# Kernel optimization log

Measured on AMD Instinct MI355X. Metric: run time of the kernel, lower is better.

The kernel has to match this reference:

```python
import jax, jax.numpy as jnp
import numpy as np

N = 100000       # nodes
E0 = 1600000     # edges without self loops
E = E0 + N       # with self loops appended (attr 0), matching add_self_loops
DIN = 128        # input_dim
HID = 64         # nb_hidden_gnn (per-head out_channels)
HEADS = 4
EMB = 128
L = 3            # nb_layer
NEG_SLOPE = 0.2
BN_EPS = 1e-5


def setup_inputs() -> dict:
    key = jax.random.key(0)
    ks = jax.random.split(key, 12)
    # edges with no self loops; self loops (i,i) appended with edge_attr 0
    row = jax.random.randint(ks[0], (E0,), 0, N)
    off = jax.random.randint(ks[1], (E0,), 1, N)
    col = (row + off) % N
    loops = jnp.arange(N, dtype=row.dtype)
    edge_index = jnp.stack([jnp.concatenate([row, loops]),
                            jnp.concatenate([col, loops])])
    edge_attr = jnp.concatenate([jax.random.normal(ks[2], (E0, 1), jnp.float32),
                                 jnp.zeros((N, 1), jnp.float32)])
    x = jax.random.normal(ks[3], (N, DIN), jnp.float32)
    HC = HEADS * HID
    linN0 = jax.random.normal(ks[4], (DIN, HC)) * HC ** -0.5
    linN_rest = jax.random.normal(ks[5], (L - 1, HID, HC)) * HC ** -0.5
    linE_all = jax.random.normal(ks[6], (L, 1, HEADS)) * HEADS ** -0.5  # nb_edge_attr=1
    att_all = jax.random.normal(ks[7], (L, HEADS, 2 * HID + 1)) * (2 * HID + 1) ** -0.5
    bias_all = jnp.zeros((L, HID))  # concat=False -> bias [out_channels]
    bn_gamma = jnp.ones((L - 1, HID))
    bn_beta = jnp.zeros((L - 1, HID))
    W = jax.random.normal(ks[8], (HID, EMB)) * HID ** -0.5
    b = jnp.zeros((EMB,))
    return {"x": x, "edge_index": edge_index, "edge_attr": edge_attr,
            "linN0": linN0, "linN_rest": linN_rest, "linE_all": linE_all,
            "att_all": att_all, "bias_all": bias_all,
            "bn_gamma": bn_gamma, "bn_beta": bn_beta, "W": W, "b": b}


def _gcn_layer(x, row, col, edge_attr, linN, linE, att, bias, bn):
    n = x.shape[0]
    if bn is not None:
        gamma, beta = bn
        mu = x.mean(axis=0)
        var = x.var(axis=0)
        x = (x - mu) * jax.lax.rsqrt(var + BN_EPS) * gamma + beta
    h = (x @ linN).reshape(n, HEADS, HID)                 # [N,H,C]
    e = (edge_attr @ linE)                                # [E,H] (nb_edge_attr=1)
    att_i = att[:, :HID]                                  # [H,C]
    att_j = att[:, HID:2 * HID]                           # [H,C]
    att_e = att[:, 2 * HID:]                              # [H,1]
    # per-node partial scores avoid gathering full features twice
    s_i = jnp.einsum('nhc,hc->nh', h, att_i)
    s_j = jnp.einsum('nhc,hc->nh', h, att_j)
    logits = s_i[row] + s_j[col] + e * att_e[:, 0]        # [E,H]
    logits = jax.nn.leaky_relu(logits, NEG_SLOPE)
    # segment softmax over destination nodes (edge_index[1])
    m = jax.ops.segment_max(logits, col, num_segments=n)
    p = jnp.exp(logits - m[col])
    denom = jax.ops.segment_sum(p, col, num_segments=n)
    alpha = p / (denom[col] + 1e-16)
    # message: alpha * x[source], scatter-add to destination
    msg = alpha[:, :, None] * h[row]                      # [E,H,C]
    out = jax.ops.segment_sum(msg, col, num_segments=n)   # [N,H,C]
    out = out.mean(axis=1) + bias + h.mean(axis=1)        # concat=False, res=True
    return jax.nn.relu(out)


def reference(x, edge_index, edge_attr, linN0, linN_rest, linE_all, att_all,
              bias_all, bn_gamma, bn_beta, W, b):
    row, col = edge_index[0], edge_index[1]
    emb = x
    for l in range(L):
        linN = linN0 if l == 0 else linN_rest[l - 1]
        bn = None if l == 0 else (bn_gamma[l - 1], bn_beta[l - 1])
        emb = _gcn_layer(emb, row, col, edge_attr, linN, linE_all[l],
                         att_all[l], bias_all[l], bn)
    return emb @ W + b
```

## Files before the change

kernel.cpp:

```cpp
#include <hip/hip_runtime.h>
#include <math.h>

#define NN 100000
#define E0E 1600000
#define EE (E0E + NN)
#define NEG 0.2f
#define BNEPS 1e-5f
#define LOG2E 1.4426950408889634f

typedef float f4 __attribute__((ext_vector_type(4)));
typedef float f2 __attribute__((ext_vector_type(2)));
typedef short s8v __attribute__((ext_vector_type(8)));

__device__ __forceinline__ float wred_max(float v) {
#pragma unroll
  for (int m = 1; m < 64; m <<= 1) v = fmaxf(v, __shfl_xor(v, m, 64));
  return v;
}
__device__ __forceinline__ float wred_sum(float v) {
#pragma unroll
  for (int m = 1; m < 64; m <<= 1) v += __shfl_xor(v, m, 64);
  return v;
}
__device__ __forceinline__ float sel4(float a0, float a1, float a2, float a3, int hd) {
  return (hd & 2) ? ((hd & 1) ? a3 : a2) : ((hd & 1) ? a1 : a0);
}
__device__ __forceinline__ unsigned short f2bf(float x) {
  unsigned u = __float_as_uint(x);
  return (unsigned short)((u + 0x7fffu + ((u >> 16) & 1u)) >> 16);
}
__device__ __forceinline__ float bf2f(unsigned short s) {
  return __uint_as_float(((unsigned)s) << 16);
}

__global__ void k_init(int* cnt, double* bnsum, int n) {
  int i = blockIdx.x * blockDim.x + threadIdx.x;
  if (i < n) cnt[i] = 0;
  if (i < 256) bnsum[i] = 0.0;
}
__global__ void k_count(const int* __restrict__ col, int* cnt, int e) {
  int i = blockIdx.x * blockDim.x + threadIdx.x;
  if (i < e) atomicAdd(&cnt[col[i]], 1);
}
#define SCAN_T 1024
__global__ void k_scan1(const int* __restrict__ cnt, int* partial, int n, int chunk) {
  int i = blockIdx.x * blockDim.x + threadIdx.x;
  int beg = i * chunk, end = min(n, beg + chunk);
  int s = 0;
  for (int j = beg; j < end; ++j) s += cnt[j];
  partial[i] = s;
}
__global__ void k_scan2(int* partial) {
  __shared__ int lds[SCAN_T];
  int t = threadIdx.x;
  int v = partial[t];
  lds[t] = v;
  __syncthreads();
  for (int off = 1; off < SCAN_T; off <<= 1) {
    int add = (t >= off) ? lds[t - off] : 0;
    __syncthreads();
    lds[t] += add;
    __syncthreads();
  }
  partial[t] = lds[t] - v;
}
__global__ void k_scan3(const int* __restrict__ cnt, const int* __restrict__ partial,
                        int* rowptr, int* cursor, int n, int chunk, int etot) {
  int i = blockIdx.x * blockDim.x + threadIdx.x;
  int beg = i * chunk, end = min(n, beg + chunk);
  int run = partial[i];
  for (int j = beg; j < end; ++j) {
    rowptr[j] = run;
    cursor[j] = run;
    run += cnt[j];
  }
  if (i == SCAN_T - 1) rowptr[n] = etot;
}
__global__ void k_scatter(const int* __restrict__ row, const int* __restrict__ col,
                          const float* __restrict__ ea, int* cursor, int2* csr, int e) {
  int i = blockIdx.x * blockDim.x + threadIdx.x;
  if (i < e) {
    int c = col[i];
    int p = atomicAdd(&cursor[c], 1);
    csr[p] = make_int2(row[i], __float_as_int(ea[i]));
  }
}

__global__ void k_bnstats(const float* __restrict__ x, double* sums, int n) {
  int f = threadIdx.x & 63;
  int rt = (blockIdx.x * blockDim.x + threadIdx.x) >> 6;
  int rstride = (gridDim.x * blockDim.x) >> 6;
  double s = 0.0, q = 0.0;
  for (int r = rt; r < n; r += rstride) {
    double v = (double)x[(size_t)r * 64 + f];
    s += v;
    q += v * v;
  }
  __shared__ double ls[256], lq[256];
  ls[threadIdx.x] = s;
  lq[threadIdx.x] = q;
  __syncthreads();
  if (threadIdx.x < 64) {
    s = ls[threadIdx.x] + ls[threadIdx.x + 64] + ls[threadIdx.x + 128] + ls[threadIdx.x + 192];
    q = lq[threadIdx.x] + lq[threadIdx.x + 64] + lq[threadIdx.x + 128] + lq[threadIdx.x + 192];
    atomicAdd(&sums[f], s);
    atomicAdd(&sums[64 + f], q);
  }
}

__global__ void k_prepw(const float* __restrict__ W, const double* __restrict__ bnsum,
                        const float* __restrict__ gamma, const float* __restrict__ beta,
                        const float* __restrict__ bin, unsigned short* __restrict__ Wt,
                        float* __restrict__ cvec, int K, int N, int mode) {
  __shared__ float ABl[128];
  int t = threadIdx.x;
  if (mode == 1) {
    if (t < 64) {
      double mean = bnsum[t] / NN;
      double var = bnsum[64 + t] / NN - mean * mean;
      float A = gamma[t] * rsqrtf((float)var + BNEPS);
      ABl[t] = A;
      ABl[64 + t] = beta[t] - (float)mean * A;
    }
    __syncthreads();
  }
  if (t >= N) return;
  float c = (mode == 2) ? bin[t] : 0.f;
  for (int k = 0; k < K; ++k) {
    float w = W[k * N + t];
    float a = 1.f, b = 0.f;
    if (mode == 1) { a = ABl[k]; b = ABl[64 + k]; }
    Wt[t * K + k] = f2bf(a * w);
    c = fmaf(b, w, c);
  }
  cvec[t] = c;
}

template <int K, int CT, bool ATT, bool OB>
__global__ __launch_bounds__(256, 2) void k_gemm(const float* __restrict__ x,
                                                 const unsigned short* __restrict__ Wt,
                                                 const float* __restrict__ cvec,
                                                 const float* __restrict__ att,
                                                 void* __restrict__ houtv,
                                                 float* __restrict__ s_i,
                                                 float* __restrict__ s_j, int n,
                                                 int ntiles) {
  constexpr int KS = K / 32;
  constexpr int ROWB = 2 * K;
  constexpr int CPR = K / 8;
  constexpr int NCOL = 4 * CT * 16;
  __shared__ unsigned char xs[64 * ROWB];
  const int lane = threadIdx.x & 63;
  const int wv = threadIdx.x >> 6;
  const int l15 = lane & 15;
  const int lq = lane >> 4;
  const int colbase = wv * CT * 16;

  s8v wfr[CT][KS];
#pragma unroll
  for (int ct = 0; ct < CT; ++ct)
#pragma unroll
    for (int ks = 0; ks < KS; ++ks)
      wfr[ct][ks] = *(const s8v*)&Wt[(size_t)(colbase + ct * 16 + l15) * K + ks * 32 + lq * 8];
  float cb[CT][4];
#pragma unroll
  for (int ct = 0; ct < CT; ++ct)
#pragma unroll
    for (int r = 0; r < 4; ++r) cb[ct][r] = cvec[colbase + ct * 16 + lq * 4 + r];
  float ati[ATT ? CT : 1][4], atj[ATT ? CT : 1][4];
  if constexpr (ATT) {
    const float* ar = att + wv * 129;
#pragma unroll
    for (int ct = 0; ct < CT; ++ct)
#pragma unroll
      for (int r = 0; r < 4; ++r) {
        int cc = ct * 16 + lq * 4 + r;
        ati[ct][r] = ar[cc];
        atj[ct][r] = ar[64 + cc];
      }
  }

  for (int t = blockIdx.x; t < ntiles; t += gridDim.x) {
    const int row0 = t * 64;
    __syncthreads();
#pragma unroll
    for (int i = 0; i < (64 * CPR) / 256; ++i) {
      int c = threadIdx.x + i * 256;
      int row = c / CPR, kc = c % CPR;
      int rg = min(row0 + row, n - 1);
      const float* xp = x + (size_t)rg * K + kc * 8;
      f4 a0 = *(const f4*)xp;
      f4 a1 = *(const f4*)(xp + 4);
      union { s8v v; unsigned short u[8]; } pk;
      pk.u[0] = f2bf(a0[0]); pk.u[1] = f2bf(a0[1]); pk.u[2] = f2bf(a0[2]); pk.u[3] = f2bf(a0[3]);
      pk.u[4] = f2bf(a1[0]); pk.u[5] = f2bf(a1[1]); pk.u[6] = f2bf(a1[2]); pk.u[7] = f2bf(a1[3]);
      *(s8v*)&xs[row * ROWB + ((kc * 16) ^ ((row & 7) << 4))] = pk.v;
    }
    __syncthreads();
    f4 acc[4][CT];
#pragma unroll
    for (int rt = 0; rt < 4; ++rt)
#pragma unroll
      for (int ct = 0; ct < CT; ++ct) acc[rt][ct] = (f4)0.f;
#pragma unroll
    for (int ks = 0; ks < KS; ++ks) {
      s8v xf[4];
#pragma unroll
      for (int rt = 0; rt < 4; ++rt) {
        int row = rt * 16 + l15;
        int kb = ks * 64 + lq * 16;
        xf[rt] = *(const s8v*)&xs[row * ROWB + (kb ^ ((row & 7) << 4))];
      }
#pragma unroll
      for (int rt = 0; rt < 4; ++rt)
#pragma unroll
        for (int ct = 0; ct < CT; ++ct)
          acc[rt][ct] = __builtin_amdgcn_mfma_f32_16x16x32_bf16(wfr[ct][ks], xf[rt],
                                                                acc[rt][ct], 0, 0, 0);
    }
#pragma unroll
    for (int rt = 0; rt < 4; ++rt) {
      if (row0 + rt * 16 >= n) continue;
      const size_t xrow = (size_t)(row0 + rt * 16 + l15);
      float v[CT][4];
#pragma unroll
      for (int ct = 0; ct < CT; ++ct)
#pragma unroll
        for (int r = 0; r < 4; ++r) v[ct][r] = acc[rt][ct][r] + cb[ct][r];
      if constexpr (OB) {
        float* outp = (float*)houtv;
#pragma unroll
        for (int ct = 0; ct < CT; ++ct) {
          f4 o;
          o[0] = v[ct][0]; o[1] = v[ct][1]; o[2] = v[ct][2]; o[3] = v[ct][3];
          *(f4*)&outp[xrow * NCOL + colbase + ct * 16 + lq * 4] = o;
        }
      } else {
        unsigned short* hout = (unsigned short*)houtv;
#pragma unroll
        for (int ct = 0; ct < CT; ++ct) {
          ushort4 hb4;
          hb4.x = f2bf(v[ct][0]); hb4.y = f2bf(v[ct][1]);
          hb4.z = f2bf(v[ct][2]); hb4.w = f2bf(v[ct][3]);
          *(ushort4*)&hout[xrow * NCOL + colbase + ct * 16 + lq * 4] = hb4;
        }
      }
      if constexpr (ATT) {
        float pi = 0.f, pj = 0.f;
#pragma unroll
        for (int ct = 0; ct < CT; ++ct)
#pragma unroll
          for (int r = 0; r < 4; ++r) {
            pi = fmaf(v[ct][r], ati[ct][r], pi);
            pj = fmaf(v[ct][r], atj[ct][r], pj);
          }
        pi += __shfl_xor(pi, 16, 64); pi += __shfl_xor(pi, 32, 64);
        pj += __shfl_xor(pj, 16, 64); pj += __shfl_xor(pj, 32, 64);
        if (lane < 16) {
          s_i[xrow * 4 + wv] = pi;
          s_j[xrow * 4 + wv] = pj;
        }
      }
    }
  }
}

template <int UNR>
__global__ __launch_bounds__(256) void k_edge(const int* __restrict__ rowptr,
                                              const int2* __restrict__ csr,
                                              const float* __restrict__ s_i,
                                              const float* __restrict__ s_j,
                                              const unsigned short* __restrict__ hb,
                                              const float* __restrict__ linE,
                                              const float* __restrict__ att,
                                              const float* __restrict__ bias,
                                              float* __restrict__ xout, int n) {
  __shared__ float lp[4][64][4];
  __shared__ int lsrc[4][64];
  const int lane = threadIdx.x & 63;
  const int wid = threadIdx.x >> 6;
  int v = blockIdx.x * 4 + wid;
  if (v >= n) return;
  v = __builtin_amdgcn_readfirstlane(v);
  const int base = rowptr[v];
  const int deg = rowptr[v + 1] - base;

  const float coef0 = linE[0] * att[0 * 129 + 128];
  const float coef1 = linE[1] * att[1 * 129 + 128];
  const float coef2 = linE[2] * att[2 * 129 + 128];
  const float coef3 = linE[3] * att[3 * 129 + 128];
  const float sj0 = s_j[(size_t)v * 4 + 0];
  const float sj1 = s_j[(size_t)v * 4 + 1];
  const float sj2 = s_j[(size_t)v * 4 + 2];
  const float sj3 = s_j[(size_t)v * 4 + 3];

  auto edge_logits = [&](int i, int& src, float& g0, float& g1, float& g2, float& g3) {
    int2 pk = csr[i];
    src = pk.x;
    float ea = __int_as_float(pk.y);
    f4 siv = *(const f4*)&s_i[(size_t)src * 4];
    g0 = siv[0] + sj0 + ea * coef0; g0 = fmaxf(g0, g0 * NEG);
    g1 = siv[1] + sj1 + ea * coef1; g1 = fmaxf(g1, g1 * NEG);
    g2 = siv[2] + sj2 + ea * coef2; g2 = fmaxf(g2, g2 * NEG);
    g3 = siv[3] + sj3 + ea * coef3; g3 = fmaxf(g3, g3 * NEG);
  };

  const int hd = lane >> 4;
  float msel, rdsel;
  bool fast = (deg <= 64);
  if (fast) {
    float g0 = -INFINITY, g1 = -INFINITY, g2 = -INFINITY, g3 = -INFINITY;
    int src = 0;
    bool valid = lane < deg;
    if (valid) edge_logits(base + lane, src, g0, g1, g2, g3);
    float m0 = wred_max(g0), m1 = wred_max(g1), m2 = wred_max(g2), m3 = wred_max(g3);
    float p0 = valid ? exp2f((g0 - m0) * LOG2E) : 0.f;
    float p1 = valid ? exp2f((g1 - m1) * LOG2E) : 0.f;
    float p2 = valid ? exp2f((g2 - m2) * LOG2E) : 0.f;
    float p3 = valid ? exp2f((g3 - m3) * LOG2E) : 0.f;
    if (valid) {
      f4 pp; pp[0] = p0; pp[1] = p1; pp[2] = p2; pp[3] = p3;
      *(f4*)&lp[wid][lane][0] = pp;
      lsrc[wid][lane] = src;
    }
    float d0 = wred_sum(p0), d1 = wred_sum(p1), d2 = wred_sum(p2), d3 = wred_sum(p3);
    rdsel = 1.f / (sel4(d0, d1, d2, d3, hd) + 1e-16f);
    msel = 0.f;
  } else {
    float m0 = -INFINITY, m1 = -INFINITY, m2 = -INFINITY, m3 = -INFINITY;
    for (int c0 = 0; c0 < deg; c0 += 64) {
      int i = c0 + lane;
      if (i < deg) {
        int src; float g0, g1, g2, g3;
        edge_logits(base + i, src, g0, g1, g2, g3);
        m0 = fmaxf(m0, g0); m1 = fmaxf(m1, g1); m2 = fmaxf(m2, g2); m3 = fmaxf(m3, g3);
      }
    }
    m0 = wred_max(m0); m1 = wred_max(m1); m2 = wred_max(m2); m3 = wred_max(m3);
    float d0 = 0, d1 = 0, d2 = 0, d3 = 0;
    for (int c0 = 0; c0 < deg; c0 += 64) {
      int i = c0 + lane;
      if (i < deg) {
        int src; float g0, g1, g2, g3;
        edge_logits(base + i, src, g0, g1, g2, g3);
        d0 += exp2f((g0 - m0) * LOG2E);
        d1 += exp2f((g1 - m1) * LOG2E);
        d2 += exp2f((g2 - m2) * LOG2E);
        d3 += exp2f((g3 - m3) * LOG2E);
      }
    }
    d0 = wred_sum(d0); d1 = wred_sum(d1); d2 = wred_sum(d2); d3 = wred_sum(d3);
    msel = sel4(m0, m1, m2, m3, hd);
    rdsel = 1.f / (sel4(d0, d1, d2, d3, hd) + 1e-16f);
  }

  f4 acc;
  {
    ushort4 hr = *(const ushort4*)&hb[(size_t)v * 256 + lane * 4];
    acc[0] = bf2f(hr.x); acc[1] = bf2f(hr.y); acc[2] = bf2f(hr.z); acc[3] = bf2f(hr.w);
  }
  if (fast) {
    int e = 0;
    if constexpr (UNR > 1) {
      for (; e + UNR <= deg; e += UNR) {
        int ss[UNR];
        float aa[UNR];
        ushort4 hh[UNR];
#pragma unroll
        for (int u = 0; u < UNR; ++u) {
          ss[u] = lsrc[wid][e + u];
          aa[u] = lp[wid][e + u][hd] * rdsel;
        }
#pragma unroll
        for (int u = 0; u < UNR; ++u)
          hh[u] = *(const ushort4*)&hb[(size_t)ss[u] * 256 + lane * 4];
#pragma unroll
        for (int u = 0; u < UNR; ++u) {
          acc[0] = fmaf(aa[u], bf2f(hh[u].x), acc[0]);
          acc[1] = fmaf(aa[u], bf2f(hh[u].y), acc[1]);
          acc[2] = fmaf(aa[u], bf2f(hh[u].z), acc[2]);
          acc[3] = fmaf(aa[u], bf2f(hh[u].w), acc[3]);
        }
      }
    }
    for (; e < deg; ++e) {
      int s0 = lsrc[wid][e];
      float a0 = lp[wid][e][hd] * rdsel;
      ushort4 h0 = *(const ushort4*)&hb[(size_t)s0 * 256 + lane * 4];
      acc[0] = fmaf(a0, bf2f(h0.x), acc[0]);
      acc[1] = fmaf(a0, bf2f(h0.y), acc[1]);
      acc[2] = fmaf(a0, bf2f(h0.z), acc[2]);
      acc[3] = fmaf(a0, bf2f(h0.w), acc[3]);
    }
  } else {
    const float sjsel = sel4(sj0, sj1, sj2, sj3, hd);
    const float cfsel = sel4(coef0, coef1, coef2, coef3, hd);
    for (int e = base; e < base + deg; ++e) {
      int2 pk = csr[e];
      int src = pk.x;
      float ea = __int_as_float(pk.y);
      f4 siv = *(const f4*)&s_i[(size_t)src * 4];
      float lg = sel4(siv[0], siv[1], siv[2], siv[3], hd) + sjsel + ea * cfsel;
      lg = fmaxf(lg, lg * NEG);
      float a = exp2f((lg - msel) * LOG2E) * rdsel;
      ushort4 hr = *(const ushort4*)&hb[(size_t)src * 256 + lane * 4];
      acc[0] = fmaf(a, bf2f(hr.x), acc[0]);
      acc[1] = fmaf(a, bf2f(hr.y), acc[1]);
      acc[2] = fmaf(a, bf2f(hr.z), acc[2]);
      acc[3] = fmaf(a, bf2f(hr.w), acc[3]);
    }
  }
#pragma unroll
  for (int m = 16; m < 64; m <<= 1) {
    acc[0] += __shfl_xor(acc[0], m, 64);
    acc[1] += __shfl_xor(acc[1], m, 64);
    acc[2] += __shfl_xor(acc[2], m, 64);
    acc[3] += __shfl_xor(acc[3], m, 64);
  }
  if (lane < 16) {
    f4 bv = *(const f4*)&bias[lane * 4];
    f4 o;
#pragma unroll
    for (int c = 0; c < 4; ++c) o[c] = fmaxf(acc[c] * 0.25f + bv[c], 0.f);
    *(f4*)&xout[(size_t)v * 64 + lane * 4] = o;
  }
}

extern "C" void kernel_launch(void* const* d_in, const int* in_sizes, int n_in,
                              void* d_out, int out_size, void* d_ws, size_t ws_size,
                              hipStream_t stream) {
  const float* x_in = (const float*)d_in[0];
  const int* ei = (const int*)d_in[1];
  const float* eattr = (const float*)d_in[2];
  const float* linN0 = (const float*)d_in[3];
  const float* linNr = (const float*)d_in[4];
  const float* linE = (const float*)d_in[5];
  const float* attA = (const float*)d_in[6];
  const float* biasA = (const float*)d_in[7];
  const float* bng = (const float*)d_in[8];
  const float* bnb = (const float*)d_in[9];
  const float* W = (const float*)d_in[10];
  const float* bb = (const float*)d_in[11];
  float* out = (float*)d_out;

  const int* row = ei;
  const int* col = ei + EE;

  char* ws = (char*)d_ws;
  size_t o = 0;
  auto alloc = [&](size_t bytes) {
    void* p = ws + o;
    o += (bytes + 255) & ~(size_t)255;
    return p;
  };
  int* cnt = (int*)alloc((size_t)NN * 4);
  int* cursor = (int*)alloc((size_t)NN * 4);
  int* rowptr = (int*)alloc((size_t)(NN + 1) * 4);
  int* partial = (int*)alloc((size_t)SCAN_T * 4);
  int2* csr = (int2*)alloc((size_t)EE * 8);
  unsigned short* h = (unsigned short*)alloc((size_t)NN * 256 * 2);
  float* si = (float*)alloc((size_t)NN * 4 * 4);
  float* sj = (float*)alloc((size_t)NN * 4 * 4);
  float* xa = (float*)alloc((size_t)NN * 64 * 4);
  float* xb = (float*)alloc((size_t)NN * 64 * 4);
  double* bnsum = (double*)alloc(256 * 8);
  unsigned short* Wt = (unsigned short*)alloc((size_t)256 * 128 * 2);
  float* cvec = (float*)alloc(256 * 4);
  if (o > ws_size) return;

  const int chunk = (NN + SCAN_T - 1) / SCAN_T;
  const int NTILES = (NN + 63) / 64;

  k_init<<<(NN + 255) / 256, 256, 0, stream>>>(cnt, bnsum, NN);
  k_count<<<(EE + 255) / 256, 256, 0, stream>>>(col, cnt, EE);
  k_scan1<<<4, 256, 0, stream>>>(cnt, partial, NN, chunk);
  k_scan2<<<1, SCAN_T, 0, stream>>>(partial);
  k_scan3<<<4, 256, 0, stream>>>(cnt, partial, rowptr, cursor, NN, chunk, EE);
  k_scatter<<<(EE + 255) / 256, 256, 0, stream>>>(row, col, eattr, cursor, csr, EE);

  k_prepw<<<1, 256, 0, stream>>>(linN0, nullptr, nullptr, nullptr, nullptr, Wt, cvec, 128, 256, 0);
  k_gemm<128, 4, true, false><<<NTILES, 256, 0, stream>>>(x_in, Wt, cvec, attA + 0, h, si, sj,
                                                          NN, NTILES);
  k_edge<4><<<NN / 4, 256, 0, stream>>>(rowptr, csr, si, sj, h, linE + 0, attA + 0, biasA + 0,
                                        xa, NN);

  k_bnstats<<<256, 256, 0, stream>>>(xa, bnsum, NN);
  k_prepw<<<1, 256, 0, stream>>>(linNr, bnsum, bng, bnb, nullptr, Wt, cvec, 64, 256, 1);
  k_gemm<64, 4, true, false><<<NTILES, 256, 0, stream>>>(xa, Wt, cvec, attA + 516, h, si, sj,
                                                         NN, NTILES);
  k_edge<2><<<NN / 4, 256, 0, stream>>>(rowptr, csr, si, sj, h, linE + 4, attA + 516, biasA + 64,
                                        xb, NN);

  k_bnstats<<<256, 256, 0, stream>>>(xb, bnsum + 128, NN);
  k_prepw<<<1, 256, 0, stream>>>(linNr + 64 * 256, bnsum + 128, bng + 64, bnb + 64, nullptr,
                                 Wt, cvec, 64, 256, 1);
  k_gemm<64, 4, true, false><<<NTILES, 256, 0, stream>>>(xb, Wt, cvec, attA + 2 * 516, h, si, sj,
                                                         NN, NTILES);
  k_edge<1><<<NN / 4, 256, 0, stream>>>(rowptr, csr, si, sj, h, linE + 8, attA + 2 * 516,
                                        biasA + 128, xa, NN);

  k_prepw<<<1, 256, 0, stream>>>(W, nullptr, nullptr, nullptr, bb, Wt, cvec, 64, 128, 2);
  k_gemm<64, 2, false, true><<<NTILES, 256, 0, stream>>>(xa, Wt, cvec, nullptr, out, nullptr,
                                                         nullptr, NN, NTILES);
}
```

Before: 904.6 us.

## Store intermediate activations in bf16, restructure edge kernel, parallelize weight prep

```diff
diff --git a/kernel.cpp b/kernel.cpp
--- a/kernel.cpp
+++ b/kernel.cpp
@@ -86,13 +86,13 @@
   }
 }
 
-__global__ void k_bnstats(const float* __restrict__ x, double* sums, int n) {
+__global__ void k_bnstats(const unsigned short* __restrict__ x, double* sums, int n) {
   int f = threadIdx.x & 63;
   int rt = (blockIdx.x * blockDim.x + threadIdx.x) >> 6;
   int rstride = (gridDim.x * blockDim.x) >> 6;
   double s = 0.0, q = 0.0;
   for (int r = rt; r < n; r += rstride) {
-    double v = (double)x[(size_t)r * 64 + f];
+    double v = (double)bf2f(x[(size_t)r * 64 + f]);
     s += v;
     q += v * v;
   }
@@ -113,6 +113,7 @@
                         const float* __restrict__ bin, unsigned short* __restrict__ Wt,
                         float* __restrict__ cvec, int K, int N, int mode) {
   __shared__ float ABl[128];
+  __shared__ float cred[4][64];
   int t = threadIdx.x;
   if (mode == 1) {
     if (t < 64) {
@@ -124,20 +125,30 @@
     }
     __syncthreads();
   }
-  if (t >= N) return;
-  float c = (mode == 2) ? bin[t] : 0.f;
-  for (int k = 0; k < K; ++k) {
-    float w = W[k * N + t];
+  int cl = t & 63, kq = t >> 6;
+  int col = blockIdx.x * 64 + cl;
+  int kn = K >> 2;
+  int k0 = kq * kn;
+  float c = 0.f;
+#pragma unroll 8
+  for (int k = k0; k < k0 + kn; ++k) {
+    float w = W[k * N + col];
     float a = 1.f, b = 0.f;
     if (mode == 1) { a = ABl[k]; b = ABl[64 + k]; }
-    Wt[t * K + k] = f2bf(a * w);
+    Wt[col * K + k] = f2bf(a * w);
     c = fmaf(b, w, c);
   }
-  cvec[t] = c;
-}
-
-template <int K, int CT, bool ATT, bool OB>
-__global__ __launch_bounds__(256, 2) void k_gemm(const float* __restrict__ x,
+  cred[kq][cl] = c;
+  __syncthreads();
+  if (kq == 0) {
+    float cc = cred[0][cl] + cred[1][cl] + cred[2][cl] + cred[3][cl];
+    if (mode == 2) cc += bin[col];
+    cvec[col] = cc;
+  }
+}
+
+template <int K, int CT, bool ATT, bool OB, bool INBF>
+__global__ __launch_bounds__(256, 2) void k_gemm(const void* __restrict__ xv,
                                                  const unsigned short* __restrict__ Wt,
                                                  const float* __restrict__ cvec,
                                                  const float* __restrict__ att,
@@ -188,13 +199,20 @@
       int c = threadIdx.x + i * 256;
       int row = c / CPR, kc = c % CPR;
       int rg = min(row0 + row, n - 1);
-      const float* xp = x + (size_t)rg * K + kc * 8;
-      f4 a0 = *(const f4*)xp;
-      f4 a1 = *(const f4*)(xp + 4);
-      union { s8v v; unsigned short u[8]; } pk;
-      pk.u[0] = f2bf(a0[0]); pk.u[1] = f2bf(a0[1]); pk.u[2] = f2bf(a0[2]); pk.u[3] = f2bf(a0[3]);
-      pk.u[4] = f2bf(a1[0]); pk.u[5] = f2bf(a1[1]); pk.u[6] = f2bf(a1[2]); pk.u[7] = f2bf(a1[3]);
-      *(s8v*)&xs[row * ROWB + ((kc * 16) ^ ((row & 7) << 4))] = pk.v;
+      int dst = row * ROWB + ((kc * 16) ^ ((row & 7) << 4));
+      if constexpr (INBF) {
+        const unsigned short* xin = (const unsigned short*)xv;
+        *(s8v*)&xs[dst] = *(const s8v*)&xin[(size_t)rg * K + kc * 8];
+      } else {
+        const float* xin = (const float*)xv;
+        const float* xp = xin + (size_t)rg * K + kc * 8;
+        f4 a0 = *(const f4*)xp;
+        f4 a1 = *(const f4*)(xp + 4);
+        union { s8v v; unsigned short u[8]; } pk;
+        pk.u[0] = f2bf(a0[0]); pk.u[1] = f2bf(a0[1]); pk.u[2] = f2bf(a0[2]); pk.u[3] = f2bf(a0[3]);
+        pk.u[4] = f2bf(a1[0]); pk.u[5] = f2bf(a1[1]); pk.u[6] = f2bf(a1[2]); pk.u[7] = f2bf(a1[3]);
+        *(s8v*)&xs[dst] = pk.v;
+      }
     }
     __syncthreads();
     f4 acc[4][CT];
@@ -265,7 +283,6 @@
   }
 }
 
-template <int UNR>
 __global__ __launch_bounds__(256) void k_edge(const int* __restrict__ rowptr,
                                               const int2* __restrict__ csr,
                                               const float* __restrict__ s_i,
@@ -274,11 +291,13 @@
                                               const float* __restrict__ linE,
                                               const float* __restrict__ att,
                                               const float* __restrict__ bias,
-                                              float* __restrict__ xout, int n) {
+                                              unsigned short* __restrict__ xout, int n) {
   __shared__ float lp[4][64][4];
   __shared__ int lsrc[4][64];
+  const unsigned char* hb8 = (const unsigned char*)hb;
   const int lane = threadIdx.x & 63;
   const int wid = threadIdx.x >> 6;
+  const int lane8 = lane * 8;
   int v = blockIdx.x * 4 + wid;
   if (v >= n) return;
   v = __builtin_amdgcn_readfirstlane(v);
@@ -306,7 +325,12 @@
   };
 
   const int hd = lane >> 4;
-  float msel, rdsel;
+  f4 acc;
+  {
+    ushort4 hr = *(const ushort4*)(hb8 + ((unsigned)v << 9) + lane8);
+    acc[0] = bf2f(hr.x); acc[1] = bf2f(hr.y); acc[2] = bf2f(hr.z); acc[3] = bf2f(hr.w);
+  }
+
   bool fast = (deg <= 64);
   if (fast) {
     float g0 = -INFINITY, g1 = -INFINITY, g2 = -INFINITY, g3 = -INFINITY;
@@ -318,14 +342,26 @@
     float p1 = valid ? exp2f((g1 - m1) * LOG2E) : 0.f;
     float p2 = valid ? exp2f((g2 - m2) * LOG2E) : 0.f;
     float p3 = valid ? exp2f((g3 - m3) * LOG2E) : 0.f;
+    float d0 = wred_sum(p0), d1 = wred_sum(p1), d2 = wred_sum(p2), d3 = wred_sum(p3);
+    float rd0 = 1.f / (d0 + 1e-16f);
+    float rd1 = 1.f / (d1 + 1e-16f);
+    float rd2 = 1.f / (d2 + 1e-16f);
+    float rd3 = 1.f / (d3 + 1e-16f);
     if (valid) {
-      f4 pp; pp[0] = p0; pp[1] = p1; pp[2] = p2; pp[3] = p3;
+      f4 pp;
+      pp[0] = p0 * rd0; pp[1] = p1 * rd1; pp[2] = p2 * rd2; pp[3] = p3 * rd3;
       *(f4*)&lp[wid][lane][0] = pp;
-      lsrc[wid][lane] = src;
-    }
-    float d0 = wred_sum(p0), d1 = wred_sum(p1), d2 = wred_sum(p2), d3 = wred_sum(p3);
-    rdsel = 1.f / (sel4(d0, d1, d2, d3, hd) + 1e-16f);
-    msel = 0.f;
+      lsrc[wid][lane] = src << 9;
+    }
+    for (int e = 0; e < deg; ++e) {
+      int off = lsrc[wid][e];
+      float a = lp[wid][e][hd];
+      ushort4 h0 = *(const ushort4*)(hb8 + (unsigned)(off + lane8));
+      acc[0] = fmaf(a, bf2f(h0.x), acc[0]);
+      acc[1] = fmaf(a, bf2f(h0.y), acc[1]);
+      acc[2] = fmaf(a, bf2f(h0.z), acc[2]);
+      acc[3] = fmaf(a, bf2f(h0.w), acc[3]);
+    }
   } else {
     float m0 = -INFINITY, m1 = -INFINITY, m2 = -INFINITY, m3 = -INFINITY;
     for (int c0 = 0; c0 < deg; c0 += 64) {
@@ -350,49 +386,8 @@
       }
     }
     d0 = wred_sum(d0); d1 = wred_sum(d1); d2 = wred_sum(d2); d3 = wred_sum(d3);
-    msel = sel4(m0, m1, m2, m3, hd);
-    rdsel = 1.f / (sel4(d0, d1, d2, d3, hd) + 1e-16f);
-  }
-
-  f4 acc;
-  {
-    ushort4 hr = *(const ushort4*)&hb[(size_t)v * 256 + lane * 4];
-    acc[0] = bf2f(hr.x); acc[1] = bf2f(hr.y); acc[2] = bf2f(hr.z); acc[3] = bf2f(hr.w);
-  }
-  if (fast) {
-    int e = 0;
-    if constexpr (UNR > 1) {
-      for (; e + UNR <= deg; e += UNR) {
-        int ss[UNR];
-        float aa[UNR];
-        ushort4 hh[UNR];
-#pragma unroll
-        for (int u = 0; u < UNR; ++u) {
-          ss[u] = lsrc[wid][e + u];
-          aa[u] = lp[wid][e + u][hd] * rdsel;
-        }
-#pragma unroll
-        for (int u = 0; u < UNR; ++u)
-          hh[u] = *(const ushort4*)&hb[(size_t)ss[u] * 256 + lane * 4];
-#pragma unroll
-        for (int u = 0; u < UNR; ++u) {
-          acc[0] = fmaf(aa[u], bf2f(hh[u].x), acc[0]);
-          acc[1] = fmaf(aa[u], bf2f(hh[u].y), acc[1]);
-          acc[2] = fmaf(aa[u], bf2f(hh[u].z), acc[2]);
-          acc[3] = fmaf(aa[u], bf2f(hh[u].w), acc[3]);
-        }
-      }
-    }
-    for (; e < deg; ++e) {
-      int s0 = lsrc[wid][e];
-      float a0 = lp[wid][e][hd] * rdsel;
-      ushort4 h0 = *(const ushort4*)&hb[(size_t)s0 * 256 + lane * 4];
-      acc[0] = fmaf(a0, bf2f(h0.x), acc[0]);
-      acc[1] = fmaf(a0, bf2f(h0.y), acc[1]);
-      acc[2] = fmaf(a0, bf2f(h0.z), acc[2]);
-      acc[3] = fmaf(a0, bf2f(h0.w), acc[3]);
-    }
-  } else {
+    float msel = sel4(m0, m1, m2, m3, hd);
+    float rdsel = 1.f / (sel4(d0, d1, d2, d3, hd) + 1e-16f);
     const float sjsel = sel4(sj0, sj1, sj2, sj3, hd);
     const float cfsel = sel4(coef0, coef1, coef2, coef3, hd);
     for (int e = base; e < base + deg; ++e) {
@@ -403,7 +398,7 @@
       float lg = sel4(siv[0], siv[1], siv[2], siv[3], hd) + sjsel + ea * cfsel;
       lg = fmaxf(lg, lg * NEG);
       float a = exp2f((lg - msel) * LOG2E) * rdsel;
-      ushort4 hr = *(const ushort4*)&hb[(size_t)src * 256 + lane * 4];
+      ushort4 hr = *(const ushort4*)(hb8 + ((unsigned)src << 9) + lane8);
       acc[0] = fmaf(a, bf2f(hr.x), acc[0]);
       acc[1] = fmaf(a, bf2f(hr.y), acc[1]);
       acc[2] = fmaf(a, bf2f(hr.z), acc[2]);
@@ -419,10 +414,12 @@
   }
   if (lane < 16) {
     f4 bv = *(const f4*)&bias[lane * 4];
-    f4 o;
-#pragma unroll
-    for (int c = 0; c < 4; ++c) o[c] = fmaxf(acc[c] * 0.25f + bv[c], 0.f);
-    *(f4*)&xout[(size_t)v * 64 + lane * 4] = o;
+    ushort4 o;
+    o.x = f2bf(fmaxf(acc[0] * 0.25f + bv[0], 0.f));
+    o.y = f2bf(fmaxf(acc[1] * 0.25f + bv[1], 0.f));
+    o.z = f2bf(fmaxf(acc[2] * 0.25f + bv[2], 0.f));
+    o.w = f2bf(fmaxf(acc[3] * 0.25f + bv[3], 0.f));
+    *(ushort4*)&xout[(size_t)v * 64 + lane * 4] = o;
   }
 }
 
@@ -461,8 +458,8 @@
   unsigned short* h = (unsigned short*)alloc((size_t)NN * 256 * 2);
   float* si = (float*)alloc((size_t)NN * 4 * 4);
   float* sj = (float*)alloc((size_t)NN * 4 * 4);
-  float* xa = (float*)alloc((size_t)NN * 64 * 4);
-  float* xb = (float*)alloc((size_t)NN * 64 * 4);
+  unsigned short* xa = (unsigned short*)alloc((size_t)NN * 64 * 2);
+  unsigned short* xb = (unsigned short*)alloc((size_t)NN * 64 * 2);
   double* bnsum = (double*)alloc(256 * 8);
   unsigned short* Wt = (unsigned short*)alloc((size_t)256 * 128 * 2);
   float* cvec = (float*)alloc(256 * 4);
@@ -470,6 +467,7 @@
 
   const int chunk = (NN + SCAN_T - 1) / SCAN_T;
   const int NTILES = (NN + 63) / 64;
+  const int GG = 391;
 
   k_init<<<(NN + 255) / 256, 256, 0, stream>>>(cnt, bnsum, NN);
   k_count<<<(EE + 255) / 256, 256, 0, stream>>>(col, cnt, EE);
@@ -478,28 +476,28 @@
   k_scan3<<<4, 256, 0, stream>>>(cnt, partial, rowptr, cursor, NN, chunk, EE);
   k_scatter<<<(EE + 255) / 256, 256, 0, stream>>>(row, col, eattr, cursor, csr, EE);
 
-  k_prepw<<<1, 256, 0, stream>>>(linN0, nullptr, nullptr, nullptr, nullptr, Wt, cvec, 128, 256, 0);
-  k_gemm<128, 4, true, false><<<NTILES, 256, 0, stream>>>(x_in, Wt, cvec, attA + 0, h, si, sj,
-                                                          NN, NTILES);
-  k_edge<4><<<NN / 4, 256, 0, stream>>>(rowptr, csr, si, sj, h, linE + 0, attA + 0, biasA + 0,
-                                        xa, NN);
+  k_prepw<<<4, 256, 0, stream>>>(linN0, nullptr, nullptr, nullptr, nullptr, Wt, cvec, 128, 256, 0);
+  k_gemm<128, 4, true, false, false><<<GG, 256, 0, stream>>>(x_in, Wt, cvec, attA + 0, h, si, sj,
+                                                             NN, NTILES);
+  k_edge<<<NN / 4, 256, 0, stream>>>(rowptr, csr, si, sj, h, linE + 0, attA + 0, biasA + 0,
+                                     xa, NN);
 
   k_bnstats<<<256, 256, 0, stream>>>(xa, bnsum, NN);
-  k_prepw<<<1, 256, 0, stream>>>(linNr, bnsum, bng, bnb, nullptr, Wt, cvec, 64, 256, 1);
-  k_gemm<64, 4, true, false><<<NTILES, 256, 0, stream>>>(xa, Wt, cvec, attA + 516, h, si, sj,
-                                                         NN, NTILES);
-  k_edge<2><<<NN / 4, 256, 0, stream>>>(rowptr, csr, si, sj, h, linE + 4, attA + 516, biasA + 64,
-                                        xb, NN);
+  k_prepw<<<4, 256, 0, stream>>>(linNr, bnsum, bng, bnb, nullptr, Wt, cvec, 64, 256, 1);
+  k_gemm<64, 4, true, false, true><<<GG, 256, 0, stream>>>(xa, Wt, cvec, attA + 516, h, si, sj,
+                                                           NN, NTILES);
+  k_edge<<<NN / 4, 256, 0, stream>>>(rowptr, csr, si, sj, h, linE + 4, attA + 516, biasA + 64,
+                                     xb, NN);
 
   k_bnstats<<<256, 256, 0, stream>>>(xb, bnsum + 128, NN);
-  k_prepw<<<1, 256, 0, stream>>>(linNr + 64 * 256, bnsum + 128, bng + 64, bnb + 64, nullptr,
+  k_prepw<<<4, 256, 0, stream>>>(linNr + 64 * 256, bnsum + 128, bng + 64, bnb + 64, nullptr,
                                  Wt, cvec, 64, 256, 1);
-  k_gemm<64, 4, true, false><<<NTILES, 256, 0, stream>>>(xb, Wt, cvec, attA + 2 * 516, h, si, sj,
-                                                         NN, NTILES);
-  k_edge<1><<<NN / 4, 256, 0, stream>>>(rowptr, csr, si, sj, h, linE + 8, attA + 2 * 516,
-                                        biasA + 128, xa, NN);
-
-  k_prepw<<<1, 256, 0, stream>>>(W, nullptr, nullptr, nullptr, bb, Wt, cvec, 64, 128, 2);
-  k_gemm<64, 2, false, true><<<NTILES, 256, 0, stream>>>(xa, Wt, cvec, nullptr, out, nullptr,
-                                                         nullptr, NN, NTILES);
-}
+  k_gemm<64, 4, true, false, true><<<GG, 256, 0, stream>>>(xb, Wt, cvec, attA + 2 * 516, h, si, sj,
+                                                           NN, NTILES);
+  k_edge<<<NN / 4, 256, 0, stream>>>(rowptr, csr, si, sj, h, linE + 8, attA + 2 * 516,
+                                     biasA + 128, xa, NN);
+
+  k_prepw<<<2, 256, 0, stream>>>(W, nullptr, nullptr, nullptr, bb, Wt, cvec, 64, 128, 2);
+  k_gemm<64, 2, false, true, true><<<GG, 256, 0, stream>>>(xa, Wt, cvec, nullptr, out, nullptr,
+                                                           nullptr, NN, NTILES);
+}
```

Result: faster. 835.7 us (-7.6%).
